# Kernel tuning notes

Measured on AMD Instinct MI355X. Metric: run time of the kernel, lower is better.

The kernel has to match this reference:

```python
import jax, jax.numpy as jnp
import numpy as np

B, N, D, DH = 8, 2048, 1024, 64

def setup_inputs() -> dict:
    key = jax.random.key(0)
    ks = jax.random.split(key, 4)
    s = 1.0 / np.sqrt(D)
    return {
        "x": jax.random.normal(ks[0], (B, N, D), dtype=jnp.float32),
        "Wq": jax.random.normal(ks[1], (D, DH), dtype=jnp.float32) * s,
        "bq": jnp.zeros((DH,), dtype=jnp.float32),
        "Wk": jax.random.normal(ks[2], (D, DH), dtype=jnp.float32) * s,
        "bk": jnp.zeros((DH,), dtype=jnp.float32),
        "Wv": jax.random.normal(ks[3], (D, DH), dtype=jnp.float32) * s,
        "bv": jnp.zeros((DH,), dtype=jnp.float32),
    }

def reference(x, Wq, bq, Wk, bk, Wv, bv):
    # Projections: [B,N,DH]
    Q = x @ Wq + bq
    K = x @ Wk + bk
    V = x @ Wv + bv
    sqrt_dh = jnp.sqrt(jnp.asarray(DH, dtype=x.dtype))
    # scores[b,i,j] = Q_i . K_j  (original materializes [B,N,N,DH]; GEMM is equivalent math)
    att = jnp.einsum("bid,bjd->bij", Q, K) / sqrt_dh
    # NOTE: original softmaxes over dim=1 (the query/i axis), not the usual j axis.
    att = jax.nn.softmax(att, axis=1)
    # Dropout is identity in eval mode.
    return jnp.einsum("bij,bjd->bid", att, V)
```

## Files before the change

kernel.cpp:

```cpp
#include <hip/hip_runtime.h>
#include <math.h>

#define Bn  8
#define Nn  2048
#define Dn  1024
#define DHn 64
#define PAD 72

typedef __attribute__((ext_vector_type(8))) short bf16x8;
typedef __attribute__((ext_vector_type(4))) float f32x4;

static __device__ inline short f2bf(float f) {
    unsigned u = __builtin_bit_cast(unsigned, f);
    u += 0x7FFFu + ((u >> 16) & 1u);
    return (short)(u >> 16);
}
static __device__ inline bf16x8 pack8(float4 a, float4 b) {
    bf16x8 v;
    v[0] = f2bf(a.x); v[1] = f2bf(a.y); v[2] = f2bf(a.z); v[3] = f2bf(a.w);
    v[4] = f2bf(b.x); v[5] = f2bf(b.y); v[6] = f2bf(b.z); v[7] = f2bf(b.w);
    return v;
}

__global__ __launch_bounds__(256) void wt_kernel(
    const float* __restrict__ Wq, const float* __restrict__ Wk,
    const float* __restrict__ Wv, short* __restrict__ Wt)
{
    const int gn = blockIdx.x;
    const float* Wm = (gn < 64) ? Wq : (gn < 128 ? Wk : Wv);
    const int n = gn & 63;
    const int t = threadIdx.x;
#pragma unroll
    for (int r = 0; r < 4; ++r) {
        const int k = t * 4 + r;
        Wt[gn * Dn + k] = f2bf(Wm[k * DHn + n]);
    }
}

__global__ __launch_bounds__(256) void qkv_kernel(
    const float* __restrict__ x, const short* __restrict__ Wt,
    const float* __restrict__ bq, const float* __restrict__ bk,
    const float* __restrict__ bv,
    short* __restrict__ Qb, short* __restrict__ Kb, short* __restrict__ Vt)
{
    __shared__ __attribute__((aligned(16))) short xs[2][32][PAD];

    const int t = threadIdx.x;
    const int w = t >> 6, lane = t & 63;
    const int c = lane & 15, quad = lane >> 4;
    const int ibase = blockIdx.x * 32;
    const int r0 = t >> 3, kc = t & 7;

    const float* xrow = &x[(size_t)(ibase + r0) * Dn + kc * 8];

    {
        const float4 a = ((const float4*)xrow)[0];
        const float4 b = ((const float4*)xrow)[1];
        *(bf16x8*)&xs[0][r0][kc * 8] = pack8(a, b);
    }

    f32x4 acc[2][3];
#pragma unroll
    for (int mt = 0; mt < 2; ++mt)
#pragma unroll
        for (int nt = 0; nt < 3; ++nt) acc[mt][nt] = (f32x4){0.f, 0.f, 0.f, 0.f};

    __syncthreads();

    for (int kt = 0; kt < 16; ++kt) {
        const int cur = kt & 1;
        bf16x8 wf[2][3];
#pragma unroll
        for (int kk = 0; kk < 2; ++kk)
#pragma unroll
            for (int nt = 0; nt < 3; ++nt)
                wf[kk][nt] = *(const bf16x8*)&Wt[(size_t)(w * 48 + nt * 16 + c) * Dn
                                                 + kt * 64 + kk * 32 + quad * 8];
        float4 pa, pb;
        if (kt < 15) {
            pa = ((const float4*)(xrow + (kt + 1) * 64))[0];
            pb = ((const float4*)(xrow + (kt + 1) * 64))[1];
        }
#pragma unroll
        for (int kk = 0; kk < 2; ++kk) {
            const bf16x8 af0 = *(const bf16x8*)&xs[cur][c][kk * 32 + quad * 8];
            const bf16x8 af1 = *(const bf16x8*)&xs[cur][16 + c][kk * 32 + quad * 8];
#pragma unroll
            for (int nt = 0; nt < 3; ++nt) {
                acc[0][nt] = __builtin_amdgcn_mfma_f32_16x16x32_bf16(af0, wf[kk][nt], acc[0][nt], 0, 0, 0);
                acc[1][nt] = __builtin_amdgcn_mfma_f32_16x16x32_bf16(af1, wf[kk][nt], acc[1][nt], 0, 0, 0);
            }
        }
        if (kt < 15) *(bf16x8*)&xs[1 - cur][r0][kc * 8] = pack8(pa, pb);
        __syncthreads();
    }

#pragma unroll
    for (int nt = 0; nt < 3; ++nt) {
        const int col = w * 48 + nt * 16 + c;
        const int mat = col >> 6, cm = col & 63;
        const float bias = (mat == 0 ? bq : (mat == 1 ? bk : bv))[cm];
#pragma unroll
        for (int mt = 0; mt < 2; ++mt) {
            if (mat == 2) {
                const int row = ibase + mt * 16 + quad * 4;
                const int b = row >> 11, i = row & (Nn - 1);
                ushort4 o;
                o.x = (unsigned short)f2bf(acc[mt][nt][0] + bias);
                o.y = (unsigned short)f2bf(acc[mt][nt][1] + bias);
                o.z = (unsigned short)f2bf(acc[mt][nt][2] + bias);
                o.w = (unsigned short)f2bf(acc[mt][nt][3] + bias);
                *(ushort4*)&Vt[((size_t)b * DHn + cm) * Nn + i] = o;
            } else {
                const float s = (mat == 1) ? 0.125f : 1.0f;
                short* Out = (mat == 0) ? Qb : Kb;
#pragma unroll
                for (int r = 0; r < 4; ++r)
                    Out[(size_t)(ibase + mt * 16 + quad * 4 + r) * DHn + cm] =
                        f2bf((acc[mt][nt][r] + bias) * s);
            }
        }
    }
}

__global__ __launch_bounds__(256) void colsum_kernel(
    const short* __restrict__ Qb, const short* __restrict__ Kb,
    float* __restrict__ lpart)
{
    __shared__ __attribute__((aligned(16))) short Qs[2][64][PAD];
    __shared__ float red[16][64];

    const int t = threadIdx.x;
    const int w = t >> 6, lane = t & 63;
    const int c = lane & 15, quad = lane >> 4;
    const int bid = blockIdx.x;
    const int b = bid >> 7, rem = bid & 127, jt = rem >> 2, s = rem & 3;
    const int jbase = jt * 64;
    const int r0 = t >> 2, cc = (t & 3) * 16;

    bf16x8 kb[4][2];
#pragma unroll
    for (int nt = 0; nt < 4; ++nt)
#pragma unroll
        for (int kk = 0; kk < 2; ++kk)
            kb[nt][kk] = *(const bf16x8*)&Kb[((size_t)b * Nn + jbase + nt * 16 + c) * DHn
                                             + kk * 32 + quad * 8];

    const short* qbase = &Qb[((size_t)b * Nn + s * 512 + r0) * DHn + cc];
    *(bf16x8*)&Qs[0][r0][cc]     = *(const bf16x8*)qbase;
    *(bf16x8*)&Qs[0][r0][cc + 8] = *(const bf16x8*)(qbase + 8);

    float lsum[4] = {0.f, 0.f, 0.f, 0.f};
    __syncthreads();

    for (int it = 0; it < 8; ++it) {
        const int cur = it & 1;
        bf16x8 p0, p1;
        if (it < 7) {
            const short* pq = qbase + (size_t)(it + 1) * 64 * DHn;
            p0 = *(const bf16x8*)pq; p1 = *(const bf16x8*)(pq + 8);
        }
        const bf16x8 aq0 = *(const bf16x8*)&Qs[cur][w * 16 + c][quad * 8];
        const bf16x8 aq1 = *(const bf16x8*)&Qs[cur][w * 16 + c][32 + quad * 8];
#pragma unroll
        for (int nt = 0; nt < 4; ++nt) {
            f32x4 sv = (f32x4){0.f, 0.f, 0.f, 0.f};
            sv = __builtin_amdgcn_mfma_f32_16x16x32_bf16(aq0, kb[nt][0], sv, 0, 0, 0);
            sv = __builtin_amdgcn_mfma_f32_16x16x32_bf16(aq1, kb[nt][1], sv, 0, 0, 0);
            lsum[nt] += __expf(sv[0]) + __expf(sv[1]) + __expf(sv[2]) + __expf(sv[3]);
        }
        if (it < 7) {
            *(bf16x8*)&Qs[1 - cur][r0][cc]     = p0;
            *(bf16x8*)&Qs[1 - cur][r0][cc + 8] = p1;
        }
        __syncthreads();
    }

#pragma unroll
    for (int nt = 0; nt < 4; ++nt) red[w * 4 + quad][nt * 16 + c] = lsum[nt];
    __syncthreads();
    if (t < 64) {
        float sum = 0.f;
#pragma unroll
        for (int r = 0; r < 16; ++r) sum += red[r][t];
        lpart[((size_t)s * Bn + b) * Nn + jbase + t] = sum;
    }
}

__global__ __launch_bounds__(256) void attnout_kernel(
    const short* __restrict__ Qb, const short* __restrict__ Kb,
    const short* __restrict__ Vt, const float* __restrict__ lpart,
    float* __restrict__ outp)
{
    __shared__ __attribute__((aligned(16))) short Ks[2][64][PAD];
    __shared__ __attribute__((aligned(16))) short Vs[2][64][PAD];
    __shared__ __attribute__((aligned(16))) short Ps[4][16][PAD];
    __shared__ float rls[2][64];

    const int t = threadIdx.x;
    const int w = t >> 6, lane = t & 63;
    const int c = lane & 15, quad = lane >> 4;
    const int bid = blockIdx.x;
    const int b = bid >> 7, rem = bid & 127, it = rem >> 2, s = rem & 3;
    const int ibase = it * 64;
    const int r0 = t >> 2, cc = (t & 3) * 16;

    const size_t qrow = (size_t)b * Nn + ibase + w * 16 + c;
    const bf16x8 aq0 = *(const bf16x8*)&Qb[qrow * DHn + quad * 8];
    const bf16x8 aq1 = *(const bf16x8*)&Qb[qrow * DHn + 32 + quad * 8];

    const short* kbase = &Kb[((size_t)b * Nn + s * 512 + r0) * DHn + cc];
    const short* vbase = &Vt[((size_t)b * DHn + r0) * Nn + s * 512 + cc];

    *(bf16x8*)&Ks[0][r0][cc]     = *(const bf16x8*)kbase;
    *(bf16x8*)&Ks[0][r0][cc + 8] = *(const bf16x8*)(kbase + 8);
    *(bf16x8*)&Vs[0][r0][cc]     = *(const bf16x8*)vbase;
    *(bf16x8*)&Vs[0][r0][cc + 8] = *(const bf16x8*)(vbase + 8);
    if (t < 64) {
        const size_t lj = (size_t)b * Nn + s * 512 + t;
        rls[0][t] = 1.0f / (lpart[lj] + lpart[(size_t)Bn * Nn + lj]
                          + lpart[2 * (size_t)Bn * Nn + lj] + lpart[3 * (size_t)Bn * Nn + lj]);
    }

    f32x4 acc[4];
#pragma unroll
    for (int dn = 0; dn < 4; ++dn) acc[dn] = (f32x4){0.f, 0.f, 0.f, 0.f};
    __syncthreads();

    for (int jt2 = 0; jt2 < 8; ++jt2) {
        const int cur = jt2 & 1;
        bf16x8 pk0, pk1, pv0, pv1; float nrl;
        if (jt2 < 7) {
            const short* pk = kbase + (size_t)(jt2 + 1) * 64 * DHn;
            pk0 = *(const bf16x8*)pk; pk1 = *(const bf16x8*)(pk + 8);
            const short* pv = vbase + (jt2 + 1) * 64;
            pv0 = *(const bf16x8*)pv; pv1 = *(const bf16x8*)(pv + 8);
            if (t < 64) {
                const size_t lj = (size_t)b * Nn + s * 512 + (jt2 + 1) * 64 + t;
                nrl = 1.0f / (lpart[lj] + lpart[(size_t)Bn * Nn + lj]
                            + lpart[2 * (size_t)Bn * Nn + lj] + lpart[3 * (size_t)Bn * Nn + lj]);
            }
        }

#pragma unroll
        for (int nt = 0; nt < 4; ++nt) {
            const bf16x8 kb0 = *(const bf16x8*)&Ks[cur][nt * 16 + c][quad * 8];
            const bf16x8 kb1 = *(const bf16x8*)&Ks[cur][nt * 16 + c][32 + quad * 8];
            f32x4 sv = (f32x4){0.f, 0.f, 0.f, 0.f};
            sv = __builtin_amdgcn_mfma_f32_16x16x32_bf16(aq0, kb0, sv, 0, 0, 0);
            sv = __builtin_amdgcn_mfma_f32_16x16x32_bf16(aq1, kb1, sv, 0, 0, 0);
            const float rl = rls[cur][nt * 16 + c];
#pragma unroll
            for (int r = 0; r < 4; ++r)
                Ps[w][quad * 4 + r][nt * 16 + c] = f2bf(__expf(sv[r]) * rl);
        }
        const bf16x8 ap0 = *(const bf16x8*)&Ps[w][c][quad * 8];
        const bf16x8 ap1 = *(const bf16x8*)&Ps[w][c][32 + quad * 8];
#pragma unroll
        for (int dn = 0; dn < 4; ++dn) {
            const bf16x8 vb0 = *(const bf16x8*)&Vs[cur][dn * 16 + c][quad * 8];
            const bf16x8 vb1 = *(const bf16x8*)&Vs[cur][dn * 16 + c][32 + quad * 8];
            acc[dn] = __builtin_amdgcn_mfma_f32_16x16x32_bf16(ap0, vb0, acc[dn], 0, 0, 0);
            acc[dn] = __builtin_amdgcn_mfma_f32_16x16x32_bf16(ap1, vb1, acc[dn], 0, 0, 0);
        }

        if (jt2 < 7) {
            *(bf16x8*)&Ks[1 - cur][r0][cc]     = pk0;
            *(bf16x8*)&Ks[1 - cur][r0][cc + 8] = pk1;
            *(bf16x8*)&Vs[1 - cur][r0][cc]     = pv0;
            *(bf16x8*)&Vs[1 - cur][r0][cc + 8] = pv1;
            if (t < 64) rls[1 - cur][t] = nrl;
        }
        __syncthreads();
    }

    float* op = outp + (size_t)s * (Bn * Nn * DHn) + ((size_t)b * Nn + ibase) * DHn;
#pragma unroll
    for (int dn = 0; dn < 4; ++dn)
#pragma unroll
        for (int r = 0; r < 4; ++r)
            op[(w * 16 + quad * 4 + r) * DHn + dn * 16 + c] = acc[dn][r];
}

__global__ __launch_bounds__(256) void outreduce_kernel(
    const float* __restrict__ outp, float* __restrict__ out)
{
    const int id = blockIdx.x * 256 + threadIdx.x;
    const float4* p = (const float4*)outp;
    const float4 a = p[id];
    const float4 b = p[id + 262144];
    const float4 c = p[id + 2 * 262144];
    const float4 d = p[id + 3 * 262144];
    float4 r;
    r.x = a.x + b.x + c.x + d.x;
    r.y = a.y + b.y + c.y + d.y;
    r.z = a.z + b.z + c.z + d.z;
    r.w = a.w + b.w + c.w + d.w;
    ((float4*)out)[id] = r;
}

extern "C" void kernel_launch(void* const* d_in, const int* in_sizes, int n_in,
                              void* d_out, int out_size, void* d_ws, size_t ws_size,
                              hipStream_t stream)
{
    const float* x  = (const float*)d_in[0];
    const float* Wq = (const float*)d_in[1];
    const float* bq = (const float*)d_in[2];
    const float* Wk = (const float*)d_in[3];
    const float* bk = (const float*)d_in[4];
    const float* Wv = (const float*)d_in[5];
    const float* bv = (const float*)d_in[6];
    float* out = (float*)d_out;

    char* ws = (char*)d_ws;
    short* Qb    = (short*)(ws);
    short* Kb    = (short*)(ws + (size_t)(1 << 21));
    short* Vt    = (short*)(ws + (size_t)(2 << 21));
    short* Wt    = (short*)(ws + (size_t)(3 << 21));
    float* lpart = (float*)(ws + (size_t)(3 << 21) + (1 << 19));
    float* outp  = (float*)(ws + (size_t)(7 << 20));

    wt_kernel<<<dim3(192), dim3(256), 0, stream>>>(Wq, Wk, Wv, Wt);
    qkv_kernel<<<dim3(512), dim3(256), 0, stream>>>(x, Wt, bq, bk, bv, Qb, Kb, Vt);
    colsum_kernel<<<dim3(1024), dim3(256), 0, stream>>>(Qb, Kb, lpart);
    attnout_kernel<<<dim3(1024), dim3(256), 0, stream>>>(Qb, Kb, Vt, lpart, outp);
    outreduce_kernel<<<dim3(1024), dim3(256), 0, stream>>>(outp, out);
}
```

Measured before the change: 171.0 us.

## Pre-swizzle weights into MFMA fragment layout and split-K QKV projection across waves

The weight transpose kernel now writes W in a fragment-ordered layout, so each lane reads its bf16x8 operand with one contiguous load. The QKV GEMM uses 16-row tiles with 128 threads, and each of its two waves handles half of the K dimension with its own private LDS x buffer, so no barriers are needed inside the loop. The two partial sums are combined through shared memory at the end. colsum also gives each wave a private Q buffer so its per-iteration __syncthreads can be dropped. The cost is extra LDS for the reduction and twice as many qkv blocks, each with more accumulator registers.

Result: slower. 214.6 us (+25.5%).

```diff
diff --git a/kernel.cpp b/kernel.cpp
--- a/kernel.cpp
+++ b/kernel.cpp
@@ -22,103 +22,109 @@
     return v;
 }
 
-__global__ __launch_bounds__(256) void wt_kernel(
+__global__ __launch_bounds__(128) void wt_kernel(
     const float* __restrict__ Wq, const float* __restrict__ Wk,
-    const float* __restrict__ Wv, short* __restrict__ Wt)
-{
-    const int gn = blockIdx.x;
-    const float* Wm = (gn < 64) ? Wq : (gn < 128 ? Wk : Wv);
-    const int n = gn & 63;
+    const float* __restrict__ Wv, short* __restrict__ Wtf)
+{
+    const int nt = blockIdx.x / 16, kt = blockIdx.x % 16;
     const int t = threadIdx.x;
-#pragma unroll
-    for (int r = 0; r < 4; ++r) {
-        const int k = t * 4 + r;
-        Wt[gn * Dn + k] = f2bf(Wm[k * DHn + n]);
-    }
-}
-
-__global__ __launch_bounds__(256) void qkv_kernel(
-    const float* __restrict__ x, const short* __restrict__ Wt,
+    const int half = t >> 6, l = t & 63;
+    const int c = l & 15, quad = l >> 4;
+    const int mat = nt >> 2, cm = (nt & 3) * 16 + c;
+    const float* Wm = (mat == 0) ? Wq : (mat == 1 ? Wk : Wv);
+    short* o = &Wtf[((((size_t)nt * 16 + kt) * 2 + half) * 64 + l) * 8];
+#pragma unroll
+    for (int e = 0; e < 8; ++e) {
+        const int k = kt * 64 + half * 32 + quad * 8 + e;
+        o[e] = f2bf(Wm[(size_t)k * DHn + cm]);
+    }
+}
+
+__global__ __launch_bounds__(128) void qkv_kernel(
+    const float* __restrict__ x, const short* __restrict__ Wtf,
     const float* __restrict__ bq, const float* __restrict__ bk,
     const float* __restrict__ bv,
     short* __restrict__ Qb, short* __restrict__ Kb, short* __restrict__ Vt)
 {
-    __shared__ __attribute__((aligned(16))) short xs[2][32][PAD];
+    __shared__ __attribute__((aligned(16))) short xs[2][2][16][PAD];
+    __shared__ f32x4 red[2][6 * 64];
 
     const int t = threadIdx.x;
-    const int w = t >> 6, lane = t & 63;
-    const int c = lane & 15, quad = lane >> 4;
-    const int ibase = blockIdx.x * 32;
-    const int r0 = t >> 3, kc = t & 7;
-
-    const float* xrow = &x[(size_t)(ibase + r0) * Dn + kc * 8];
+    const int w = t >> 6, l = t & 63;
+    const int c = l & 15, quad = l >> 4;
+    const int ibase = blockIdx.x * 16;
+    const int srow = l >> 2, scol = (l & 3) * 16;
+
+    const float* xbase = &x[(size_t)(ibase + srow) * Dn + w * 512 + scol];
 
     {
-        const float4 a = ((const float4*)xrow)[0];
-        const float4 b = ((const float4*)xrow)[1];
-        *(bf16x8*)&xs[0][r0][kc * 8] = pack8(a, b);
-    }
-
-    f32x4 acc[2][3];
-#pragma unroll
-    for (int mt = 0; mt < 2; ++mt)
-#pragma unroll
-        for (int nt = 0; nt < 3; ++nt) acc[mt][nt] = (f32x4){0.f, 0.f, 0.f, 0.f};
-
+        const float4* p = (const float4*)xbase;
+        *(bf16x8*)&xs[w][0][srow][scol]     = pack8(p[0], p[1]);
+        *(bf16x8*)&xs[w][0][srow][scol + 8] = pack8(p[2], p[3]);
+    }
+
+    f32x4 acc[12];
+#pragma unroll
+    for (int nt = 0; nt < 12; ++nt) acc[nt] = (f32x4){0.f, 0.f, 0.f, 0.f};
+
+    for (int kt = 0; kt < 8; ++kt) {
+        const int cur = kt & 1;
+        float4 p0, p1, p2, p3;
+        if (kt < 7) {
+            const float4* p = (const float4*)(xbase + (kt + 1) * 64);
+            p0 = p[0]; p1 = p[1]; p2 = p[2]; p3 = p[3];
+        }
+        const int ktg = w * 8 + kt;
+#pragma unroll
+        for (int h = 0; h < 2; ++h) {
+            const bf16x8 af = *(const bf16x8*)&xs[w][cur][c][h * 32 + quad * 8];
+            const short* wrow = &Wtf[(((size_t)ktg * 2 + h) * 64 + l) * 8];
+#pragma unroll
+            for (int nt = 0; nt < 12; ++nt) {
+                const bf16x8 bf = *(const bf16x8*)&wrow[(size_t)nt * 16 * 2 * 64 * 8];
+                acc[nt] = __builtin_amdgcn_mfma_f32_16x16x32_bf16(af, bf, acc[nt], 0, 0, 0);
+            }
+        }
+        if (kt < 7) {
+            *(bf16x8*)&xs[w][1 - cur][srow][scol]     = pack8(p0, p1);
+            *(bf16x8*)&xs[w][1 - cur][srow][scol + 8] = pack8(p2, p3);
+        }
+    }
+
+#pragma unroll
+    for (int q = 0; q < 6; ++q) {
+        const int nt = (w == 0) ? (6 + q) : q;
+        red[w][q * 64 + l] = acc[nt];
+    }
     __syncthreads();
-
-    for (int kt = 0; kt < 16; ++kt) {
-        const int cur = kt & 1;
-        bf16x8 wf[2][3];
-#pragma unroll
-        for (int kk = 0; kk < 2; ++kk)
-#pragma unroll
-            for (int nt = 0; nt < 3; ++nt)
-                wf[kk][nt] = *(const bf16x8*)&Wt[(size_t)(w * 48 + nt * 16 + c) * Dn
-                                                 + kt * 64 + kk * 32 + quad * 8];
-        float4 pa, pb;
-        if (kt < 15) {
-            pa = ((const float4*)(xrow + (kt + 1) * 64))[0];
-            pb = ((const float4*)(xrow + (kt + 1) * 64))[1];
-        }
-#pragma unroll
-        for (int kk = 0; kk < 2; ++kk) {
-            const bf16x8 af0 = *(const bf16x8*)&xs[cur][c][kk * 32 + quad * 8];
-            const bf16x8 af1 = *(const bf16x8*)&xs[cur][16 + c][kk * 32 + quad * 8];
-#pragma unroll
-            for (int nt = 0; nt < 3; ++nt) {
-                acc[0][nt] = __builtin_amdgcn_mfma_f32_16x16x32_bf16(af0, wf[kk][nt], acc[0][nt], 0, 0, 0);
-                acc[1][nt] = __builtin_amdgcn_mfma_f32_16x16x32_bf16(af1, wf[kk][nt], acc[1][nt], 0, 0, 0);
-            }
-        }
-        if (kt < 15) *(bf16x8*)&xs[1 - cur][r0][kc * 8] = pack8(pa, pb);
-        __syncthreads();
-    }
-
-#pragma unroll
-    for (int nt = 0; nt < 3; ++nt) {
-        const int col = w * 48 + nt * 16 + c;
-        const int mat = col >> 6, cm = col & 63;
+#pragma unroll
+    for (int q = 0; q < 6; ++q) {
+        const int nt = w * 6 + q;
+        const f32x4 o = red[1 - w][q * 64 + l];
+        acc[nt][0] += o[0]; acc[nt][1] += o[1]; acc[nt][2] += o[2]; acc[nt][3] += o[3];
+    }
+
+    const int b = ibase >> 11;
+#pragma unroll
+    for (int q = 0; q < 6; ++q) {
+        const int nt = w * 6 + q;
+        const int mat = nt >> 2, cm = (nt & 3) * 16 + c;
         const float bias = (mat == 0 ? bq : (mat == 1 ? bk : bv))[cm];
-#pragma unroll
-        for (int mt = 0; mt < 2; ++mt) {
-            if (mat == 2) {
-                const int row = ibase + mt * 16 + quad * 4;
-                const int b = row >> 11, i = row & (Nn - 1);
-                ushort4 o;
-                o.x = (unsigned short)f2bf(acc[mt][nt][0] + bias);
-                o.y = (unsigned short)f2bf(acc[mt][nt][1] + bias);
-                o.z = (unsigned short)f2bf(acc[mt][nt][2] + bias);
-                o.w = (unsigned short)f2bf(acc[mt][nt][3] + bias);
-                *(ushort4*)&Vt[((size_t)b * DHn + cm) * Nn + i] = o;
-            } else {
-                const float s = (mat == 1) ? 0.125f : 1.0f;
-                short* Out = (mat == 0) ? Qb : Kb;
-#pragma unroll
-                for (int r = 0; r < 4; ++r)
-                    Out[(size_t)(ibase + mt * 16 + quad * 4 + r) * DHn + cm] =
-                        f2bf((acc[mt][nt][r] + bias) * s);
-            }
+        if (mat == 2) {
+            const int i = (ibase & (Nn - 1)) + quad * 4;
+            ushort4 o;
+            o.x = (unsigned short)f2bf(acc[nt][0] + bias);
+            o.y = (unsigned short)f2bf(acc[nt][1] + bias);
+            o.z = (unsigned short)f2bf(acc[nt][2] + bias);
+            o.w = (unsigned short)f2bf(acc[nt][3] + bias);
+            *(ushort4*)&Vt[((size_t)b * DHn + cm) * Nn + i] = o;
+        } else {
+            const float s = (mat == 1) ? 0.125f : 1.0f;
+            short* Out = (mat == 0) ? Qb : Kb;
+#pragma unroll
+            for (int r = 0; r < 4; ++r)
+                Out[(size_t)(ibase + quad * 4 + r) * DHn + cm] =
+                    f2bf((acc[nt][r] + bias) * s);
         }
     }
 }
@@ -127,16 +133,16 @@
     const short* __restrict__ Qb, const short* __restrict__ Kb,
     float* __restrict__ lpart)
 {
-    __shared__ __attribute__((aligned(16))) short Qs[2][64][PAD];
+    __shared__ __attribute__((aligned(16))) short Qw[4][2][16][PAD];
     __shared__ float red[16][64];
 
     const int t = threadIdx.x;
-    const int w = t >> 6, lane = t & 63;
-    const int c = lane & 15, quad = lane >> 4;
+    const int w = t >> 6, l = t & 63;
+    const int c = l & 15, quad = l >> 4;
     const int bid = blockIdx.x;
     const int b = bid >> 7, rem = bid & 127, jt = rem >> 2, s = rem & 3;
     const int jbase = jt * 64;
-    const int r0 = t >> 2, cc = (t & 3) * 16;
+    const int srow = l >> 2, scol = (l & 3) * 16;
 
     bf16x8 kb[4][2];
 #pragma unroll
@@ -146,22 +152,22 @@
             kb[nt][kk] = *(const bf16x8*)&Kb[((size_t)b * Nn + jbase + nt * 16 + c) * DHn
                                              + kk * 32 + quad * 8];
 
-    const short* qbase = &Qb[((size_t)b * Nn + s * 512 + r0) * DHn + cc];
-    *(bf16x8*)&Qs[0][r0][cc]     = *(const bf16x8*)qbase;
-    *(bf16x8*)&Qs[0][r0][cc + 8] = *(const bf16x8*)(qbase + 8);
+    const short* qbase = &Qb[((size_t)b * Nn + s * 512 + w * 16 + srow) * DHn + scol];
+
+    *(bf16x8*)&Qw[w][0][srow][scol]     = *(const bf16x8*)qbase;
+    *(bf16x8*)&Qw[w][0][srow][scol + 8] = *(const bf16x8*)(qbase + 8);
 
     float lsum[4] = {0.f, 0.f, 0.f, 0.f};
-    __syncthreads();
-
-    for (int it = 0; it < 8; ++it) {
-        const int cur = it & 1;
+
+    for (int ch = 0; ch < 8; ++ch) {
+        const int cur = ch & 1;
         bf16x8 p0, p1;
-        if (it < 7) {
-            const short* pq = qbase + (size_t)(it + 1) * 64 * DHn;
+        if (ch < 7) {
+            const short* pq = qbase + (size_t)(ch + 1) * 64 * DHn;
             p0 = *(const bf16x8*)pq; p1 = *(const bf16x8*)(pq + 8);
         }
-        const bf16x8 aq0 = *(const bf16x8*)&Qs[cur][w * 16 + c][quad * 8];
-        const bf16x8 aq1 = *(const bf16x8*)&Qs[cur][w * 16 + c][32 + quad * 8];
+        const bf16x8 aq0 = *(const bf16x8*)&Qw[w][cur][c][quad * 8];
+        const bf16x8 aq1 = *(const bf16x8*)&Qw[w][cur][c][32 + quad * 8];
 #pragma unroll
         for (int nt = 0; nt < 4; ++nt) {
             f32x4 sv = (f32x4){0.f, 0.f, 0.f, 0.f};
@@ -169,11 +175,10 @@
             sv = __builtin_amdgcn_mfma_f32_16x16x32_bf16(aq1, kb[nt][1], sv, 0, 0, 0);
             lsum[nt] += __expf(sv[0]) + __expf(sv[1]) + __expf(sv[2]) + __expf(sv[3]);
         }
-        if (it < 7) {
-            *(bf16x8*)&Qs[1 - cur][r0][cc]     = p0;
-            *(bf16x8*)&Qs[1 - cur][r0][cc + 8] = p1;
-        }
-        __syncthreads();
+        if (ch < 7) {
+            *(bf16x8*)&Qw[w][1 - cur][srow][scol]     = p0;
+            *(bf16x8*)&Qw[w][1 - cur][srow][scol + 8] = p1;
+        }
     }
 
 #pragma unroll
@@ -316,12 +321,12 @@
     short* Qb    = (short*)(ws);
     short* Kb    = (short*)(ws + (size_t)(1 << 21));
     short* Vt    = (short*)(ws + (size_t)(2 << 21));
-    short* Wt    = (short*)(ws + (size_t)(3 << 21));
+    short* Wtf   = (short*)(ws + (size_t)(3 << 21));
     float* lpart = (float*)(ws + (size_t)(3 << 21) + (1 << 19));
     float* outp  = (float*)(ws + (size_t)(7 << 20));
 
-    wt_kernel<<<dim3(192), dim3(256), 0, stream>>>(Wq, Wk, Wv, Wt);
-    qkv_kernel<<<dim3(512), dim3(256), 0, stream>>>(x, Wt, bq, bk, bv, Qb, Kb, Vt);
+    wt_kernel<<<dim3(192), dim3(128), 0, stream>>>(Wq, Wk, Wv, Wtf);
+    qkv_kernel<<<dim3(1024), dim3(128), 0, stream>>>(x, Wtf, bq, bk, bv, Qb, Kb, Vt);
     colsum_kernel<<<dim3(1024), dim3(256), 0, stream>>>(Qb, Kb, lpart);
     attnout_kernel<<<dim3(1024), dim3(256), 0, stream>>>(Qb, Kb, Vt, lpart, outp);
     outreduce_kernel<<<dim3(1024), dim3(256), 0, stream>>>(outp, out);
```
